# Kernel tuning notes

Measured on AMD Instinct MI355X. Metric: run time of the kernel, lower is better.

Reference implementation:

```python
import math
import jax, jax.numpy as jnp
import numpy as np

B, T, D, N = 4, 4096, 2048, 512
FACIL_RATE = 2.0
FIRE_THRESH = 0.85
MAX_GATE = 8.0
EPS = 1e-12  # F.normalize eps


def _gelu(x):
    c = math.sqrt(2.0 / math.pi)
    return 0.5 * x * (1.0 + jnp.tanh(c * (x + 0.044715 * x ** 3)))


def _normalize(v, axis=-1):
    n = jnp.linalg.norm(v, axis=axis, keepdims=True)
    return v / jnp.maximum(n, EPS)


def setup_inputs() -> dict:
    key = jax.random.key(0)
    k1, k2, k3 = jax.random.split(key, 3)
    return {
        "x": jax.random.normal(k1, (B, T, D), dtype=jnp.float32),
        "log_k_mag": jnp.asarray(math.log(0.5), dtype=jnp.float32),
        "keys": jax.random.normal(k2, (N, D), dtype=jnp.float32),
        "mag": jax.random.uniform(k3, (N, D), dtype=jnp.float32, minval=0.1, maxval=1.0),
        "facil": jnp.full((N,), 2.0, dtype=jnp.float32),
        "mask": jnp.ones((N,), dtype=bool),
    }


def reference(x, log_k_mag, keys, mag, facil, mask):
    Bb, Tt, Dd = x.shape
    k_mag = jnp.clip(jnp.exp(log_k_mag), 0.01, 5.0)
    y = _gelu(x)  # [B,T,D]
    # torch detaches y before the buffer math
    y_flat = jax.lax.stop_gradient(y.reshape(Bb * Tt, Dd))
    y_mean = y_flat.mean(0)  # [D]
    m_n = _normalize(y_mean, axis=0)
    keys_n = _normalize(keys)  # [N,D]
    sims = jnp.where(mask, keys_n @ m_n, -1.0)  # [N]
    idx = jnp.argmax(sims)
    fire = sims[idx] > FIRE_THRESH
    facil_level = jnp.where(fire, facil[idx] * FACIL_RATE, facil[idx])
    mag_vec = mag[idx]  # [D]
    importance = mag_vec / jnp.maximum(mag_vec.mean(), 1e-6)
    mv_n = keys_n[idx]  # [D] (already L2-normalized key)
    y_n = _normalize(y_flat)  # [B*T, D]
    tok_sim = jnp.clip(y_n @ mv_n, 0.0, 1.0).reshape(Bb, Tt, 1)
    gate_d = jnp.minimum(1.0 + k_mag * (facil_level - 1.0) * importance, MAX_GATE)  # [D]
    gate = gate_d.reshape(1, 1, Dd) * tok_sim + (1.0 - tok_sim)
    return y * gate
```

## Files before the change

kernel.cpp:

```cpp
#include <hip/hip_runtime.h>
#include <math.h>

#define ROWS 16384
#define D    2048
#define NKEYS 512
#define PBLK 1024

__device__ inline float gelu1(float v) {
    float t = 0.7978845608028654f * fmaf(0.044715f * v, v * v, v);
    float e = __expf(2.0f * t);
    return v * (1.0f - 1.0f / (e + 1.0f));
}

__device__ inline float4 gelu4(float4 v) {
    float4 r;
    r.x = gelu1(v.x); r.y = gelu1(v.y); r.z = gelu1(v.z); r.w = gelu1(v.w);
    return r;
}

__device__ inline void block_reduce_sum2(float& a, float& b) {
    __shared__ float sa[4], sb[4];
    for (int off = 32; off; off >>= 1) {
        a += __shfl_down(a, off, 64);
        b += __shfl_down(b, off, 64);
    }
    const int lane = threadIdx.x & 63, w = threadIdx.x >> 6;
    if (lane == 0) { sa[w] = a; sb[w] = b; }
    __syncthreads();
    if (threadIdx.x == 0) {
        a = sa[0] + sa[1] + sa[2] + sa[3];
        b = sb[0] + sb[1] + sb[2] + sb[3];
        sa[0] = a; sb[0] = b;
    }
    __syncthreads();
    a = sa[0]; b = sb[0];
    __syncthreads();
}

__global__ __launch_bounds__(256) void colsum_kernel(const float* __restrict__ x,
                                                     float* __restrict__ partials) {
    const int t = threadIdx.x;
    float4 a0 = {0.f,0.f,0.f,0.f}, a1 = {0.f,0.f,0.f,0.f};
    for (int row = blockIdx.x; row < ROWS; row += PBLK) {
        const float4* xr = (const float4*)(x + (size_t)row * D);
        float4 y0 = gelu4(xr[t]);
        float4 y1 = gelu4(xr[t + 256]);
        a0.x += y0.x; a0.y += y0.y; a0.z += y0.z; a0.w += y0.w;
        a1.x += y1.x; a1.y += y1.y; a1.z += y1.z; a1.w += y1.w;
    }
    float4* pr = (float4*)(partials + (size_t)blockIdx.x * D);
    pr[t]       = a0;
    pr[t + 256] = a1;
}

__global__ __launch_bounds__(256) void reduce_kernel(const float* __restrict__ partials,
                                                     float* __restrict__ colsum) {
    const int c = blockIdx.x;
    const int t = threadIdx.x;
    float s = 0.f, dummy = 0.f;
    #pragma unroll
    for (int k = 0; k < PBLK / 256; ++k) {
        s += partials[(size_t)(t + 256 * k) * D + c];
    }
    block_reduce_sum2(s, dummy);
    if (t == 0) colsum[c] = s;
}

__global__ __launch_bounds__(256) void sims_kernel(const float* __restrict__ keys,
                                                   const float* __restrict__ colsum,
                                                   float* __restrict__ sims) {
    const int i = blockIdx.x;
    const int t = threadIdx.x;
    const float4* kr = (const float4*)(keys + (size_t)i * D);
    const float4* s4 = (const float4*)colsum;
    float4 k0 = kr[t], k1 = kr[t + 256];
    float4 c0 = s4[t], c1 = s4[t + 256];
    float dot = k0.x*c0.x + k0.y*c0.y + k0.z*c0.z + k0.w*c0.w
              + k1.x*c1.x + k1.y*c1.y + k1.z*c1.z + k1.w*c1.w;
    float ksq = k0.x*k0.x + k0.y*k0.y + k0.z*k0.z + k0.w*k0.w
              + k1.x*k1.x + k1.y*k1.y + k1.z*k1.z + k1.w*k1.w;
    block_reduce_sum2(dot, ksq);
    if (t == 0) sims[i] = dot / fmaxf(sqrtf(ksq), 1e-12f);
}

__global__ __launch_bounds__(256) void finalize_kernel(const float* __restrict__ colsum,
                                                       const float* __restrict__ sims,
                                                       const float* __restrict__ keys,
                                                       const float* __restrict__ mag,
                                                       const float* __restrict__ facil,
                                                       const float* __restrict__ logk,
                                                       float* __restrict__ gate_d,
                                                       float* __restrict__ mv_n) {
    const int t = threadIdx.x;
    __shared__ float sv[256];
    __shared__ int   si[256];
    __shared__ int   s_idx;
    __shared__ float s_val;

    float best = -3.402823466e38f; int bidx = 0;
    for (int i = t; i < NKEYS; i += 256) {
        float v = sims[i];
        if (v > best) { best = v; bidx = i; }
    }
    sv[t] = best; si[t] = bidx;
    __syncthreads();
    if (t == 0) {
        float bv = sv[0]; int bi = si[0];
        for (int i = 1; i < 256; i++) {
            if (sv[i] > bv || (sv[i] == bv && si[i] < bi)) { bv = sv[i]; bi = si[i]; }
        }
        s_idx = bi; s_val = bv;
    }
    __syncthreads();
    const int idx = s_idx;

    float ss = 0.f, dummy = 0.f;
    for (int d = t; d < D; d += 256) { float v = colsum[d]; ss += v * v; }
    block_reduce_sum2(ss, dummy);
    const float normS = fmaxf(sqrtf(ss), 1e-12f);
    const float true_sim = s_val / normS;
    const bool fire = true_sim > 0.85f;

    const float fl = facil[idx] * (fire ? 2.0f : 1.0f);
    const float km = fminf(fmaxf(expf(logk[0]), 0.01f), 5.0f);

    const float* mrow = mag  + (size_t)idx * D;
    const float* krow = keys + (size_t)idx * D;
    float msum = 0.f, ksq = 0.f;
    for (int d = t; d < D; d += 256) {
        msum += mrow[d];
        float k = krow[d];
        ksq += k * k;
    }
    block_reduce_sum2(msum, ksq);
    const float mmean = fmaxf(msum / (float)D, 1e-6f);
    const float knorm = fmaxf(sqrtf(ksq), 1e-12f);
    const float coef = km * (fl - 1.0f) / mmean;

    for (int d = t; d < D; d += 256) {
        gate_d[d] = fminf(fmaf(coef, mrow[d], 1.0f), 8.0f);
        mv_n[d]   = krow[d] / knorm;
    }
}

__global__ __launch_bounds__(256) void main_kernel(const float* __restrict__ x,
                                                   const float* __restrict__ gate_d,
                                                   const float* __restrict__ mv_n,
                                                   float* __restrict__ out) {
    const int row = blockIdx.x;
    const int t = threadIdx.x;
    const float4* xr = (const float4*)(x + (size_t)row * D);
    float4 y0 = gelu4(xr[t]);
    float4 y1 = gelu4(xr[t + 256]);

    const float4* mv4 = (const float4*)mv_n;
    float4 m0 = mv4[t], m1 = mv4[t + 256];

    float dot = y0.x*m0.x + y0.y*m0.y + y0.z*m0.z + y0.w*m0.w
              + y1.x*m1.x + y1.y*m1.y + y1.z*m1.z + y1.w*m1.w;
    float ss  = y0.x*y0.x + y0.y*y0.y + y0.z*y0.z + y0.w*y0.w
              + y1.x*y1.x + y1.y*y1.y + y1.z*y1.z + y1.w*y1.w;
    block_reduce_sum2(dot, ss);

    float ts = dot / fmaxf(sqrtf(ss), 1e-12f);
    ts = fminf(fmaxf(ts, 0.0f), 1.0f);
    const float omts = 1.0f - ts;

    const float4* g4 = (const float4*)gate_d;
    float4 g0 = g4[t], g1 = g4[t + 256];

    float4 o0, o1;
    o0.x = y0.x * fmaf(g0.x, ts, omts);
    o0.y = y0.y * fmaf(g0.y, ts, omts);
    o0.z = y0.z * fmaf(g0.z, ts, omts);
    o0.w = y0.w * fmaf(g0.w, ts, omts);
    o1.x = y1.x * fmaf(g1.x, ts, omts);
    o1.y = y1.y * fmaf(g1.y, ts, omts);
    o1.z = y1.z * fmaf(g1.z, ts, omts);
    o1.w = y1.w * fmaf(g1.w, ts, omts);

    float4* outr = (float4*)(out + (size_t)row * D);
    outr[t]       = o0;
    outr[t + 256] = o1;
}

extern "C" void kernel_launch(void* const* d_in, const int* in_sizes, int n_in,
                              void* d_out, int out_size, void* d_ws, size_t ws_size,
                              hipStream_t stream) {
    const float* x     = (const float*)d_in[0];
    const float* logk  = (const float*)d_in[1];
    const float* keys  = (const float*)d_in[2];
    const float* mag   = (const float*)d_in[3];
    const float* facil = (const float*)d_in[4];
    float* out = (float*)d_out;

    float* ws       = (float*)d_ws;
    float* colsum   = ws;
    float* sims     = ws + 2048;
    float* gate_d   = ws + 2560;
    float* mv_n     = ws + 4608;
    float* partials = ws + 6656;

    colsum_kernel  <<<PBLK, 256, 0, stream>>>(x, partials);
    reduce_kernel  <<<D, 256, 0, stream>>>(partials, colsum);
    sims_kernel    <<<NKEYS, 256, 0, stream>>>(keys, colsum, sims);
    finalize_kernel<<<1, 256, 0, stream>>>(colsum, sims, keys, mag, facil, logk, gate_d, mv_n);
    main_kernel    <<<ROWS, 256, 0, stream>>>(x, gate_d, mv_n, out);
}
```

Measured before the change: 114.2 us.

## Give colsum blocks contiguous row chunks and coalesce the partial-sum reduction

The column-sum pass now gives each of 2048 blocks 8 contiguous rows and issues 8 float4 loads before doing any GELU work, which adds memory-level parallelism. The reduce kernel now handles 16 columns per block with 16 row groups, so reads of the partials array are partly coalesced and far fewer blocks are launched. The finalize kernel now uses vectorized float4 loads and stores and multiplies by a precomputed reciprocal norm. In exchange the partials buffer doubles in size, which adds traffic between the two kernels.

Result: no change. 115.4 us (+1.0%).

```diff
diff --git a/kernel.cpp b/kernel.cpp
--- a/kernel.cpp
+++ b/kernel.cpp
@@ -4,7 +4,8 @@
 #define ROWS 16384
 #define D    2048
 #define NKEYS 512
-#define PBLK 1024
+#define PBLK 2048
+#define RPB  (ROWS / PBLK)
 
 __device__ inline float gelu1(float v) {
     float t = 0.7978845608028654f * fmaf(0.044715f * v, v * v, v);
@@ -16,6 +17,10 @@
     float4 r;
     r.x = gelu1(v.x); r.y = gelu1(v.y); r.z = gelu1(v.z); r.w = gelu1(v.w);
     return r;
+}
+
+__device__ inline void acc4(float4& a, float4 v) {
+    a.x += v.x; a.y += v.y; a.z += v.z; a.w += v.w;
 }
 
 __device__ inline void block_reduce_sum2(float& a, float& b) {
@@ -40,13 +45,23 @@
 __global__ __launch_bounds__(256) void colsum_kernel(const float* __restrict__ x,
                                                      float* __restrict__ partials) {
     const int t = threadIdx.x;
+    const float4* xb = (const float4*)(x + (size_t)blockIdx.x * RPB * D);
     float4 a0 = {0.f,0.f,0.f,0.f}, a1 = {0.f,0.f,0.f,0.f};
-    for (int row = blockIdx.x; row < ROWS; row += PBLK) {
-        const float4* xr = (const float4*)(x + (size_t)row * D);
-        float4 y0 = gelu4(xr[t]);
-        float4 y1 = gelu4(xr[t + 256]);
-        a0.x += y0.x; a0.y += y0.y; a0.z += y0.z; a0.w += y0.w;
-        a1.x += y1.x; a1.y += y1.y; a1.z += y1.z; a1.w += y1.w;
+    #pragma unroll
+    for (int r = 0; r < RPB; r += 4) {
+        const int b = r * (D / 4);
+        float4 v0 = xb[b + 0*(D/4) + t];
+        float4 w0 = xb[b + 0*(D/4) + t + 256];
+        float4 v1 = xb[b + 1*(D/4) + t];
+        float4 w1 = xb[b + 1*(D/4) + t + 256];
+        float4 v2 = xb[b + 2*(D/4) + t];
+        float4 w2 = xb[b + 2*(D/4) + t + 256];
+        float4 v3 = xb[b + 3*(D/4) + t];
+        float4 w3 = xb[b + 3*(D/4) + t + 256];
+        acc4(a0, gelu4(v0)); acc4(a1, gelu4(w0));
+        acc4(a0, gelu4(v1)); acc4(a1, gelu4(w1));
+        acc4(a0, gelu4(v2)); acc4(a1, gelu4(w2));
+        acc4(a0, gelu4(v3)); acc4(a1, gelu4(w3));
     }
     float4* pr = (float4*)(partials + (size_t)blockIdx.x * D);
     pr[t]       = a0;
@@ -55,15 +70,24 @@
 
 __global__ __launch_bounds__(256) void reduce_kernel(const float* __restrict__ partials,
                                                      float* __restrict__ colsum) {
-    const int c = blockIdx.x;
-    const int t = threadIdx.x;
-    float s = 0.f, dummy = 0.f;
-    #pragma unroll
-    for (int k = 0; k < PBLK / 256; ++k) {
-        s += partials[(size_t)(t + 256 * k) * D + c];
-    }
-    block_reduce_sum2(s, dummy);
-    if (t == 0) colsum[c] = s;
+    const int t = threadIdx.x;
+    const int cidx = t & 15;
+    const int rg   = t >> 4;
+    const int c = blockIdx.x * 16 + cidx;
+    float s = 0.f;
+    #pragma unroll 8
+    for (int r = rg; r < PBLK; r += 16) {
+        s += partials[(size_t)r * D + c];
+    }
+    __shared__ float sm[256];
+    sm[t] = s;
+    __syncthreads();
+    if (t < 16) {
+        float acc = 0.f;
+        #pragma unroll
+        for (int k = 0; k < 16; ++k) acc += sm[t + 16 * k];
+        colsum[blockIdx.x * 16 + t] = acc;
+    }
 }
 
 __global__ __launch_bounds__(256) void sims_kernel(const float* __restrict__ keys,
@@ -124,23 +148,37 @@
     const float fl = facil[idx] * (fire ? 2.0f : 1.0f);
     const float km = fminf(fmaxf(expf(logk[0]), 0.01f), 5.0f);
 
-    const float* mrow = mag  + (size_t)idx * D;
-    const float* krow = keys + (size_t)idx * D;
-    float msum = 0.f, ksq = 0.f;
-    for (int d = t; d < D; d += 256) {
-        msum += mrow[d];
-        float k = krow[d];
-        ksq += k * k;
-    }
+    const float4* mrow4 = (const float4*)(mag  + (size_t)idx * D);
+    const float4* krow4 = (const float4*)(keys + (size_t)idx * D);
+    float4 mA = mrow4[t], mB = mrow4[t + 256];
+    float4 kA = krow4[t], kB = krow4[t + 256];
+    float msum = mA.x + mA.y + mA.z + mA.w + mB.x + mB.y + mB.z + mB.w;
+    float ksq  = kA.x*kA.x + kA.y*kA.y + kA.z*kA.z + kA.w*kA.w
+               + kB.x*kB.x + kB.y*kB.y + kB.z*kB.z + kB.w*kB.w;
     block_reduce_sum2(msum, ksq);
     const float mmean = fmaxf(msum / (float)D, 1e-6f);
     const float knorm = fmaxf(sqrtf(ksq), 1e-12f);
     const float coef = km * (fl - 1.0f) / mmean;
-
-    for (int d = t; d < D; d += 256) {
-        gate_d[d] = fminf(fmaf(coef, mrow[d], 1.0f), 8.0f);
-        mv_n[d]   = krow[d] / knorm;
-    }
+    const float rkn = 1.0f / knorm;
+
+    float4 gA, gB, nA, nB;
+    gA.x = fminf(fmaf(coef, mA.x, 1.0f), 8.0f);
+    gA.y = fminf(fmaf(coef, mA.y, 1.0f), 8.0f);
+    gA.z = fminf(fmaf(coef, mA.z, 1.0f), 8.0f);
+    gA.w = fminf(fmaf(coef, mA.w, 1.0f), 8.0f);
+    gB.x = fminf(fmaf(coef, mB.x, 1.0f), 8.0f);
+    gB.y = fminf(fmaf(coef, mB.y, 1.0f), 8.0f);
+    gB.z = fminf(fmaf(coef, mB.z, 1.0f), 8.0f);
+    gB.w = fminf(fmaf(coef, mB.w, 1.0f), 8.0f);
+    nA.x = kA.x * rkn; nA.y = kA.y * rkn; nA.z = kA.z * rkn; nA.w = kA.w * rkn;
+    nB.x = kB.x * rkn; nB.y = kB.y * rkn; nB.z = kB.z * rkn; nB.w = kB.w * rkn;
+
+    float4* g4 = (float4*)gate_d;
+    float4* n4 = (float4*)mv_n;
+    g4[t]       = gA;
+    g4[t + 256] = gB;
+    n4[t]       = nA;
+    n4[t + 256] = nB;
 }
 
 __global__ __launch_bounds__(256) void main_kernel(const float* __restrict__ x,
@@ -202,7 +240,7 @@
     float* partials = ws + 6656;
 
     colsum_kernel  <<<PBLK, 256, 0, stream>>>(x, partials);
-    reduce_kernel  <<<D, 256, 0, stream>>>(partials, colsum);
+    reduce_kernel  <<<D / 16, 256, 0, stream>>>(partials, colsum);
     sims_kernel    <<<NKEYS, 256, 0, stream>>>(keys, colsum, sims);
     finalize_kernel<<<1, 256, 0, stream>>>(colsum, sims, keys, mag, facil, logk, gate_d, mv_n);
     main_kernel    <<<ROWS, 256, 0, stream>>>(x, gate_d, mv_n, out);
```
